# Performance work log

Hardware: AMD Instinct MI355X
Metric: run time of the kernel (lower is better)

## Reference

```python
import jax, jax.numpy as jnp
import numpy as np

N_FREQ = 128
N_SPACE = 3
DIS_DIM = 2 * N_FREQ * N_SPACE  # 768


def sin_emb(x):
    # x: [E, 3] -> [E, 768]; frequencies = 2*pi*arange(n_freq) as in DiffCSP SinusoidsEmbedding
    freq = 2.0 * jnp.pi * jnp.arange(N_FREQ, dtype=x.dtype)
    e = (x[..., None] * freq).reshape(x.shape[0], N_SPACE * N_FREQ)
    return jnp.concatenate([jnp.sin(e), jnp.cos(e)], axis=-1)


def layer_norm(x, g, b, eps=1e-5):
    m = jnp.mean(x, axis=-1, keepdims=True)
    v = jnp.var(x, axis=-1, keepdims=True)
    return (x - m) * jax.lax.rsqrt(v + eps) * g + b


def setup_inputs() -> dict:
    key = jax.random.key(0)
    ks = jax.random.split(key, 16)
    N, E, B, H = 10000, 200000, 50, 512
    E_IN = 2 * H + DIS_DIM + 6  # 1798
    s = 0.02
    return {
        "node_features": jax.random.normal(ks[0], (N, H), jnp.float32),
        "lattices": jax.random.normal(ks[1], (B, 6), jnp.float32),
        "edge_index": jax.random.randint(ks[2], (2, E), 0, N),
        "edge2graph": jax.random.randint(ks[3], (E,), 0, B),
        "frac_diff": jax.random.uniform(ks[4], (E, 3), jnp.float32),
        "num_atoms": jax.random.randint(ks[5], (B,), 1, 200),
        "ln_gamma": jnp.ones((H,), jnp.float32),
        "ln_beta": jnp.zeros((H,), jnp.float32),
        "W_e1": jax.random.normal(ks[6], (E_IN, H), jnp.float32) * s,
        "b_e1": jnp.zeros((H,), jnp.float32),
        "W_e2": jax.random.normal(ks[7], (H, H), jnp.float32) * s,
        "b_e2": jnp.zeros((H,), jnp.float32),
        "W_n1": jax.random.normal(ks[8], (2 * H, H), jnp.float32) * s,
        "b_n1": jnp.zeros((H,), jnp.float32),
        "W_n2": jax.random.normal(ks[9], (H, H), jnp.float32) * s,
        "b_n2": jnp.zeros((H,), jnp.float32),
    }


def reference(node_features, lattices, edge_index, edge2graph, frac_diff, num_atoms,
              ln_gamma, ln_beta, W_e1, b_e1, W_e2, b_e2, W_n1, b_n1, W_n2, b_n2):
    N = node_features.shape[0]
    # pre-LN (ln=True): residual uses raw input
    h = layer_norm(node_features, ln_gamma, ln_beta)
    # edge model: gather + concat + 2-layer MLP with SiLU
    hi = h[edge_index[0]]
    hj = h[edge_index[1]]
    fd = sin_emb(frac_diff)
    lat_e = lattices.reshape(lattices.shape[0], -1)[edge2graph]
    e_in = jnp.concatenate([hi, hj, lat_e, fd], axis=1)  # [E, 1798]
    e = jax.nn.silu(e_in @ W_e1 + b_e1)
    e = jax.nn.silu(e @ W_e2 + b_e2)
    # node model: scatter-mean over edge source + 2-layer MLP
    agg = jax.ops.segment_sum(e, edge_index[0], num_segments=N)
    cnt = jax.ops.segment_sum(jnp.ones((e.shape[0],), e.dtype), edge_index[0], num_segments=N)
    agg = agg / jnp.maximum(cnt, 1.0)[:, None]
    n_in = jnp.concatenate([h, agg], axis=1)  # [N, 1024]
    o = jax.nn.silu(n_in @ W_n1 + b_n1)
    o = jax.nn.silu(o @ W_n2 + b_n2)
    return node_features + o
```

## Files before the change

### kernel.cpp

```cpp
#include <hip/hip_runtime.h>
#include <hip/hip_bf16.h>


#include <type_traits>

typedef __attribute__((ext_vector_type(8))) short bfrag;
typedef __attribute__((ext_vector_type(4))) float ffrag;

#define DEVI __device__ __forceinline__

constexpr int N_NODES = 10000;
constexpr int N_EDGES = 200000;
constexpr int HD      = 512;
constexpr int NT      = HD / 16;
constexpr int SLABW   = 520;
constexpr int KSTR    = NT * 64 * 8;

DEVI float silu_f(float v) { return v / (1.0f + __expf(-v)); }

DEVI ushort f2bf(float f) {
    unsigned u = __float_as_uint(f);
    unsigned r = (u + 0x7fffu + ((u >> 16) & 1u)) >> 16;
    return (ushort)r;
}
DEVI float bf2f(ushort v) { return __uint_as_float((unsigned)v << 16); }

DEVI int cperm(int col) {
    return (col & ~63) | ((col & 15) << 2) | ((col >> 4) & 3);
}

__global__ void wswz_kernel(const float* __restrict__ W, ushort* __restrict__ dst,
                            int Kp, int mode) {
    int fid = blockIdx.x * blockDim.x + threadIdx.x;
    int total = (Kp / 32) * NT * 64;
    if (fid >= total) return;
    int l  = fid & 63;
    int nn = (fid >> 6) & 31;
    int kk = fid >> 11;
    int col = nn * 16 + (l & 15);
    int kb  = kk * 32 + (l >> 4) * 8;
    union { ushort u16[8]; uint4 u4; } v;
    for (int j = 0; j < 8; ++j) {
        int krow = kb + j;
        int src;
        if (mode == 3) {
            int d = krow >> 8, rm = krow & 255, k = rm >> 1;
            src = ((rm & 1) ? 1414 : 1030) + d * 128 + k;
        } else {
            src = krow;
        }
        v.u16[j] = f2bf(W[(size_t)src * HD + col]);
    }
    *(uint4*)(dst + (size_t)fid * 8) = v.u4;
}

__global__ void ln_kernel(const float* __restrict__ x, const float* __restrict__ g,
                          const float* __restrict__ b, ushort* __restrict__ h) {
    __shared__ float wred[8];
    __shared__ float mb[2];
    int row = blockIdx.x;
    int t = threadIdx.x;
    const float* xr = x + (size_t)row * HD;
    float x0 = xr[t], x1 = xr[t + 256];
    float s = x0 + x1, q = x0 * x0 + x1 * x1;
    for (int o = 32; o; o >>= 1) { s += __shfl_down(s, o); q += __shfl_down(q, o); }
    int w = t >> 6, l = t & 63;
    if (l == 0) { wred[w] = s; wred[w + 4] = q; }
    __syncthreads();
    if (t == 0) {
        float S = wred[0] + wred[1] + wred[2] + wred[3];
        float Q = wred[4] + wred[5] + wred[6] + wred[7];
        float m = S * (1.0f / HD);
        float v = Q * (1.0f / HD) - m * m;
        mb[0] = m; mb[1] = rsqrtf(v + 1e-5f);
    }
    __syncthreads();
    float m = mb[0], rs = mb[1];
    h[(size_t)row * HD + t]       = f2bf((x0 - m) * rs * g[t] + b[t]);
    h[(size_t)row * HD + t + 256] = f2bf((x1 - m) * rs * g[t + 256] + b[t + 256]);
}

__global__ void latb_kernel(const float* __restrict__ latt, const float* __restrict__ W_e1,
                            const float* __restrict__ b1, float* __restrict__ LATBp) {
    int g = blockIdx.x;
    int t = threadIdx.x;
    float a = b1[t];
    for (int c = 0; c < 6; ++c)
        a += latt[g * 6 + c] * W_e1[(size_t)(1024 + c) * HD + t];
    LATBp[(size_t)g * HD + cperm(t)] = a;
}

__global__ void zero_kernel(int* __restrict__ c32, float* __restrict__ agg) {
    int i = blockIdx.x * 256 + threadIdx.x;
    if (i < N_NODES) c32[i] = 0;
    agg[i] = 0.0f;
}

__global__ void hist_kernel(const int* __restrict__ eidx, int* __restrict__ cnt32) {
    int e = blockIdx.x * 256 + threadIdx.x;
    if (e < N_EDGES) atomicAdd(&cnt32[eidx[e]], 1);
}

__global__ void scan_kernel(const int* __restrict__ cnt32, int* __restrict__ row_ptr,
                            int* __restrict__ cursor) {
    __shared__ int buf[1024];
    int t = threadIdx.x;
    int base = t * 10;
    int loc[10]; int s = 0;
    for (int i = 0; i < 10; ++i) {
        int idx = base + i;
        int v = (idx < N_NODES) ? cnt32[idx] : 0;
        loc[i] = s; s += v;
    }
    buf[t] = s; __syncthreads();
    for (int off = 1; off < 1024; off <<= 1) {
        int v = 0; if (t >= off) v = buf[t - off];
        __syncthreads();
        buf[t] += v; __syncthreads();
    }
    int excl = buf[t] - s;
    for (int i = 0; i < 10; ++i) {
        int idx = base + i;
        if (idx < N_NODES) { int p = excl + loc[i]; row_ptr[idx] = p; cursor[idx] = p; }
    }
    if (t == 0) row_ptr[N_NODES] = N_EDGES;
}

__global__ void csr_fill(const int* __restrict__ eidx, int* __restrict__ cursor,
                         int* __restrict__ ebuf) {
    int e = blockIdx.x * 256 + threadIdx.x;
    if (e >= N_EDGES) return;
    int pos = atomicAdd(&cursor[eidx[e]], 1);
    ebuf[pos] = e;
}

__global__ void aggdiv_kernel(const float* __restrict__ agg, const int* __restrict__ rp,
                              ushort* __restrict__ aggb) {
    int i = blockIdx.x * 256 + threadIdx.x;
    int row = i >> 9;
    int deg = rp[row + 1] - rp[row];
    float rc = 1.0f / (float)max(deg, 1);
    aggb[i] = f2bf(agg[i] * rc);
}

__global__ void sentinel_kernel(float* o, int n) {
    int i = blockIdx.x * 256 + threadIdx.x;
    if (i < n) o[i] = 123456789.0f;
}

template <int KTN, int MT>
DEVI void kloop_rot(ffrag (&acc)[MT][4], const ushort* sl, const ushort* bp0,
                    int ml, int q) {
    bfrag b_[4];
    const ushort* bp = bp0;
    #pragma unroll
    for (int n = 0; n < 4; ++n) b_[n] = *(const bfrag*)(bp + n * 512);
    #pragma unroll
    for (int p = 0; p < KTN; ++p) {
        bfrag a_[MT];
        #pragma unroll
        for (int m = 0; m < MT; ++m)
            a_[m] = *(const bfrag*)&sl[(16 * m + ml) * SLABW + p * 32 + q * 8];
        const ushort* bpn = bp + KSTR;
        #pragma unroll
        for (int n = 0; n < 4; ++n) {
            #pragma unroll
            for (int m = 0; m < MT; ++m)
                acc[m][n] = __builtin_amdgcn_mfma_f32_16x16x32_bf16(a_[m], b_[n], acc[m][n], 0, 0, 0);
            if (p + 1 < KTN) b_[n] = *(const bfrag*)(bpn + n * 512);
        }
        bp = bpn;
    }
}

__global__ __launch_bounds__(512, 4) void hab_gemm(
    const ushort* __restrict__ h, const ushort* __restrict__ w1a_s,
    const ushort* __restrict__ w1b_s, ushort* __restrict__ HAp,
    ushort* __restrict__ HBp) {

    __shared__ __align__(16) ushort slab[32 * SLABW];
    const int t = threadIdx.x;
    const int w = t >> 6;
    const int l = t & 63;
    const int q = l >> 4;
    const int ml = l & 15;
    const int rowbase = blockIdx.x * 32;
    const ushort* Bswz = blockIdx.y ? w1b_s : w1a_s;
    ushort* out = blockIdx.y ? HBp : HAp;

    for (int j = 0; j < 4; ++j) {
        int rr = w * 4 + j;
        int row = rowbase + rr;
        if (row >= N_NODES) row = N_NODES - 1;
        *(uint4*)&slab[rr * SLABW + l * 8] =
            *(const uint4*)(h + (size_t)row * HD + l * 8);
    }
    __syncthreads();

    ffrag acc[2][4];
    for (int m = 0; m < 2; ++m)
        for (int n = 0; n < 4; ++n)
            acc[m][n] = (ffrag){0.f, 0.f, 0.f, 0.f};

    kloop_rot<16, 2>(acc, slab, Bswz + ((size_t)(w << 2) * 64 + l) * 8, ml, q);

    for (int m = 0; m < 2; ++m)
        for (int rr = 0; rr < 4; ++rr) {
            int grow = rowbase + 16 * m + 4 * q + rr;
            if (grow < N_NODES) {
                ushort4 v = make_ushort4(f2bf(acc[m][0][rr]), f2bf(acc[m][1][rr]),
                                         f2bf(acc[m][2][rr]), f2bf(acc[m][3][rr]));
                *(ushort4*)(out + (size_t)grow * HD + w * 64 + ml * 4) = v;
            }
        }
}

__global__ __launch_bounds__(512, 4) void edge_mlp(
    const ushort* __restrict__ HAp,   const ushort* __restrict__ HBp,
    const float* __restrict__ LATBp,  const ushort* __restrict__ w1c,
    const ushort* __restrict__ w2s,   const float* __restrict__ b2,
    float* __restrict__ agg,
    const int* __restrict__ edge_index, const int* __restrict__ e2g,
    const float* __restrict__ frac_diff, const int* __restrict__ ebuf) {

    __shared__ __align__(16) ushort slab[64 * SLABW];
    __shared__ int   ssrc[64];
    __shared__ int   sdst[64];
    __shared__ int   sgrp[64];
    __shared__ float sfd[64 * 3];

    const int t = threadIdx.x;
    const int w = t >> 6;
    const int l = t & 63;
    const int q = l >> 4;
    const int ml = l & 15;
    const int rowbase = blockIdx.x * 64;

    if (t < 64) {
        int eid = ebuf[rowbase + t];
        ssrc[t] = edge_index[eid];
        sdst[t] = edge_index[N_EDGES + eid];
        sgrp[t] = e2g[eid];
        for (int c = 0; c < 3; ++c) sfd[t * 3 + c] = frac_diff[(size_t)eid * 3 + c];
    }
    __syncthreads();

    ffrag acc[4][4];
    {
        const int cb = w * 64 + ml * 4;
        for (int m = 0; m < 4; ++m)
            for (int rr = 0; rr < 4; ++rr) {
                int rowl = 16 * m + 4 * q + rr;
                ushort4 a4 = *(const ushort4*)(HAp + (size_t)ssrc[rowl] * HD + cb);
                ushort4 h4 = *(const ushort4*)(HBp + (size_t)sdst[rowl] * HD + cb);
                float4  l4 = *(const float4*)(LATBp + (size_t)sgrp[rowl] * HD + cb);
                acc[m][0][rr] = bf2f(a4.x) + bf2f(h4.x) + l4.x;
                acc[m][1][rr] = bf2f(a4.y) + bf2f(h4.y) + l4.y;
                acc[m][2][rr] = bf2f(a4.z) + bf2f(h4.z) + l4.z;
                acc[m][3][rr] = bf2f(a4.w) + bf2f(h4.w) + l4.w;
            }
    }

    const int r  = t >> 3;
    const int c0 = (t & 7) * 4;
    float fd3[3] = { sfd[r * 3 + 0], sfd[r * 3 + 1], sfd[r * 3 + 2] };

    auto stage = [&](int phase) {
        for (int i = 0; i < 12; ++i) {
            int c = c0 + 32 * i;
            int cp = phase * 384 + c;
            int d = cp >> 8;
            float x = fd3[d];
            int k0 = (cp & 255) >> 1;
            float f0 = (float)k0 * x;
            float f1 = f0 + x;
            float r0 = __builtin_amdgcn_fractf(f0);
            float r1 = __builtin_amdgcn_fractf(f1);
            union { __hip_bfloat162 h2[2]; ushort4 u4; } pk;
            pk.h2[0] = __float22bfloat162_rn(float2{__builtin_amdgcn_sinf(r0),
                                                    __builtin_amdgcn_cosf(r0)});
            pk.h2[1] = __float22bfloat162_rn(float2{__builtin_amdgcn_sinf(r1),
                                                    __builtin_amdgcn_cosf(r1)});
            *(ushort4*)&slab[r * SLABW + c] = pk.u4;
        }
    };

    const ushort* bpw1 = w1c + ((size_t)(w << 2) * 64 + l) * 8;
    const ushort* bpw2 = w2s + ((size_t)(w << 2) * 64 + l) * 8;

    stage(0);
    __syncthreads();
    kloop_rot<12, 4>(acc, slab, bpw1, ml, q);
    __syncthreads();
    stage(1);
    __syncthreads();
    kloop_rot<12, 4>(acc, slab, bpw1 + (size_t)12 * KSTR, ml, q);
    __syncthreads();

    for (int n = 0; n < 4; ++n) {
        int cg = w * 64 + n * 16 + ml;
        for (int m = 0; m < 4; ++m)
            for (int rr = 0; rr < 4; ++rr) {
                int rowl = 16 * m + 4 * q + rr;
                slab[rowl * SLABW + cg] = f2bf(silu_f(acc[m][n][rr]));
            }
    }
    for (int m = 0; m < 4; ++m)
        for (int n = 0; n < 4; ++n)
            acc[m][n] = (ffrag){0.f, 0.f, 0.f, 0.f};
    __syncthreads();

    kloop_rot<16, 4>(acc, slab, bpw2, ml, q);

    float* fs = (float*)slab;
    for (int hh = 0; hh < 2; ++hh) {
        __syncthreads();
        if ((w >> 2) == hh) {
            for (int n = 0; n < 4; ++n) {
                int cg = w * 64 + n * 16 + ml;
                int lc = cg - hh * 256;
                float bv = b2[cg];
                for (int m = 0; m < 4; ++m)
                    for (int rr = 0; rr < 4; ++rr) {
                        int rowl = 16 * m + 4 * q + rr;
                        fs[rowl * 256 + lc] = silu_f(acc[m][n][rr] + bv);
                    }
            }
        }
        __syncthreads();
        if (t < 256) {
            int col = hh * 256 + t;
            int cur = ssrc[0];
            float run = 0.f;
            for (int rr2 = 0; rr2 < 64; ++rr2) {
                int nd = ssrc[rr2];
                if (nd != cur) {
                    unsafeAtomicAdd(&agg[(size_t)cur * HD + col], run);
                    run = 0.f; cur = nd;
                }
                run += fs[rr2 * 256 + t];
            }
            unsafeAtomicAdd(&agg[(size_t)cur * HD + col], run);
        }
    }
}

__global__ __launch_bounds__(512, 4) void node_mlp(
    const ushort* __restrict__ h,     const ushort* __restrict__ aggb,
    const ushort* __restrict__ wn1s,  const ushort* __restrict__ wn2s,
    const float* __restrict__ b1,     const float* __restrict__ b2,
    const float* __restrict__ nf,     float* __restrict__ out) {

    __shared__ __align__(16) ushort slab[64 * SLABW];

    const int t = threadIdx.x;
    const int w = t >> 6;
    const int l = t & 63;
    const int q = l >> 4;
    const int ml = l & 15;
    const int rowbase = blockIdx.x * 64;

    ffrag acc[4][4];
    for (int m = 0; m < 4; ++m)
        for (int n = 0; n < 4; ++n)
            acc[m][n] = (ffrag){0.f, 0.f, 0.f, 0.f};

    auto load_rows = [&](const ushort* base) {
        for (int j = 0; j < 8; ++j) {
            int rr = w * 8 + j;
            int row = rowbase + rr;
            if (row >= N_NODES) row = N_NODES - 1;
            *(uint4*)&slab[rr * SLABW + l * 8] =
                *(const uint4*)(base + (size_t)row * HD + l * 8);
        }
    };
    const ushort* bp1 = wn1s + ((size_t)(w << 2) * 64 + l) * 8;
    const ushort* bp2 = wn2s + ((size_t)(w << 2) * 64 + l) * 8;

    load_rows(h);                        __syncthreads();
    kloop_rot<16, 4>(acc, slab, bp1, ml, q);
    __syncthreads();
    load_rows(aggb);                     __syncthreads();
    kloop_rot<16, 4>(acc, slab, bp1 + (size_t)16 * KSTR, ml, q);
    __syncthreads();

    for (int n = 0; n < 4; ++n) {
        int cg = w * 64 + n * 16 + ml;
        float bv = b1[cg];
        for (int m = 0; m < 4; ++m)
            for (int rr = 0; rr < 4; ++rr) {
                int rowl = 16 * m + 4 * q + rr;
                slab[rowl * SLABW + cg] = f2bf(silu_f(acc[m][n][rr] + bv));
            }
    }
    for (int m = 0; m < 4; ++m)
        for (int n = 0; n < 4; ++n)
            acc[m][n] = (ffrag){0.f, 0.f, 0.f, 0.f};
    __syncthreads();

    kloop_rot<16, 4>(acc, slab, bp2, ml, q);

    for (int n = 0; n < 4; ++n) {
        int cg = w * 64 + n * 16 + ml;
        float bv = b2[cg];
        for (int m = 0; m < 4; ++m)
            for (int rr = 0; rr < 4; ++rr) {
                int rowl = 16 * m + 4 * q + rr;
                int row = rowbase + rowl;
                if (row < N_NODES) {
                    float v = silu_f(acc[m][n][rr] + bv);
                    out[(size_t)row * HD + cg] = nf[(size_t)row * HD + cg] + v;
                }
            }
    }
}

extern "C" void kernel_launch(void* const* d_in, const int* in_sizes, int n_in,
                              void* d_out, int out_size, void* d_ws, size_t ws_size,
                              hipStream_t stream) {
    const float* nf      = (const float*)d_in[0];
    const float* latt    = (const float*)d_in[1];
    const int*   eidx    = (const int*)d_in[2];
    const int*   e2g     = (const int*)d_in[3];
    const float* fd      = (const float*)d_in[4];
    const float* ln_g    = (const float*)d_in[6];
    const float* ln_b    = (const float*)d_in[7];
    const float* W_e1    = (const float*)d_in[8];
    const float* b_e1    = (const float*)d_in[9];
    const float* W_e2    = (const float*)d_in[10];
    const float* b_e2    = (const float*)d_in[11];
    const float* W_n1    = (const float*)d_in[12];
    const float* b_n1    = (const float*)d_in[13];
    const float* W_n2    = (const float*)d_in[14];
    const float* b_n2    = (const float*)d_in[15];
    float* out = (float*)d_out;

    auto al = [](size_t x) { return (x + 511) & ~(size_t)511; };
    size_t off_h    = 0;                         size_t sz_h    = (size_t)N_NODES * HD * 2;
    size_t off_w1a  = al(off_h + sz_h);          size_t sz_w1a  = (size_t)HD * HD * 2;
    size_t off_w1b  = al(off_w1a + sz_w1a);      size_t sz_w1b  = (size_t)HD * HD * 2;
    size_t off_w1c  = al(off_w1b + sz_w1b);      size_t sz_w1c  = (size_t)768 * HD * 2;
    size_t off_w2   = al(off_w1c + sz_w1c);      size_t sz_w2   = (size_t)HD * HD * 2;
    size_t off_wn1  = al(off_w2 + sz_w2);        size_t sz_wn1  = (size_t)2 * HD * HD * 2;
    size_t off_wn2  = al(off_wn1 + sz_wn1);      size_t sz_wn2  = (size_t)HD * HD * 2;
    size_t off_ha   = al(off_wn2 + sz_wn2);      size_t sz_ha   = (size_t)N_NODES * HD * 2;
    size_t off_hb   = al(off_ha + sz_ha);        size_t sz_hb   = (size_t)N_NODES * HD * 2;
    size_t off_lb   = al(off_hb + sz_hb);        size_t sz_lb   = (size_t)50 * HD * 4;
    size_t off_agb  = al(off_lb + sz_lb);        size_t sz_agb  = (size_t)N_NODES * HD * 2;
    size_t off_c32  = al(off_agb + sz_agb);      size_t sz_c32  = (size_t)N_NODES * 4;
    size_t off_cur  = al(off_c32 + sz_c32);      size_t sz_cur  = (size_t)N_NODES * 4;
    size_t off_rp   = al(off_cur + sz_cur);      size_t sz_rp   = (size_t)(N_NODES + 1) * 4;
    size_t off_ebuf = al(off_rp + sz_rp);        size_t sz_ebuf = (size_t)N_EDGES * 4;
    size_t off_agg  = al(off_ebuf + sz_ebuf);    size_t sz_agg  = (size_t)N_NODES * HD * 4;
    size_t need     = off_agg + sz_agg;

    if (ws_size < need) {
        sentinel_kernel<<<(out_size + 255) / 256, 256, 0, stream>>>(out, out_size);
        return;
    }

    char* ws = (char*)d_ws;
    ushort* h     = (ushort*)(ws + off_h);
    ushort* w1a_s = (ushort*)(ws + off_w1a);
    ushort* w1b_s = (ushort*)(ws + off_w1b);
    ushort* w1c_s = (ushort*)(ws + off_w1c);
    ushort* w2s   = (ushort*)(ws + off_w2);
    ushort* wn1s  = (ushort*)(ws + off_wn1);
    ushort* wn2s  = (ushort*)(ws + off_wn2);
    ushort* HAp   = (ushort*)(ws + off_ha);
    ushort* HBp   = (ushort*)(ws + off_hb);
    float*  LATBp = (float*)(ws + off_lb);
    ushort* aggb  = (ushort*)(ws + off_agb);
    int*    c32   = (int*)(ws + off_c32);
    int*    cur   = (int*)(ws + off_cur);
    int*    rp    = (int*)(ws + off_rp);
    int*    ebuf  = (int*)(ws + off_ebuf);
    float*  agg   = (float*)(ws + off_agg);

    zero_kernel<<<(N_NODES * HD) / 256, 256, 0, stream>>>(c32, agg);
    wswz_kernel<<<(HD / 32) * NT * 64 / 256, 256, 0, stream>>>(W_e1, w1a_s, HD, 0);
    wswz_kernel<<<(HD / 32) * NT * 64 / 256, 256, 0, stream>>>(W_e1 + (size_t)HD * HD, w1b_s, HD, 0);
    wswz_kernel<<<(768 / 32) * NT * 64 / 256, 256, 0, stream>>>(W_e1, w1c_s, 768, 3);
    wswz_kernel<<<(HD / 32) * NT * 64 / 256, 256, 0, stream>>>(W_e2, w2s, HD, 0);
    wswz_kernel<<<(2 * HD / 32) * NT * 64 / 256, 256, 0, stream>>>(W_n1, wn1s, 2 * HD, 0);
    wswz_kernel<<<(HD / 32) * NT * 64 / 256, 256, 0, stream>>>(W_n2, wn2s, HD, 0);
    latb_kernel<<<50, 512, 0, stream>>>(latt, W_e1, b_e1, LATBp);

    hist_kernel<<<(N_EDGES + 255) / 256, 256, 0, stream>>>(eidx, c32);
    scan_kernel<<<1, 1024, 0, stream>>>(c32, rp, cur);
    csr_fill<<<(N_EDGES + 255) / 256, 256, 0, stream>>>(eidx, cur, ebuf);

    ln_kernel<<<N_NODES, 256, 0, stream>>>(nf, ln_g, ln_b, h);
    hab_gemm<<<dim3(313, 2), 512, 0, stream>>>(h, w1a_s, w1b_s, HAp, HBp);

    edge_mlp<<<N_EDGES / 64, 512, 0, stream>>>(
        HAp, HBp, LATBp, w1c_s, w2s, b_e2, agg, eidx, e2g, fd, ebuf);

    aggdiv_kernel<<<(N_NODES * HD) / 256, 256, 0, stream>>>(agg, rp, aggb);

    int nblocks = (N_NODES + 63) / 64;
    node_mlp<<<nblocks, 512, 0, stream>>>(h, aggb, wn1s, wn2s, b_n1, b_n2, nf, out);
}
```

Measured before the change: 610.0 us.

## Vectorize small kernels, use trig recurrence for sinusoid embedding, shrink node tiles

Several unrelated tweaks land together. The LN, zero and aggdiv kernels now use vectorized loads and stores, and the SiLU epilogues write packed 4-wide bf16 stores, with the K-row permutation of W_e2 and W_n2 changed to match. The sinusoid embedding in edge_mlp replaces per-element sin/cos calls with an angle-addition recurrence. node_mlp moves to 32-row tiles so the 10000 nodes spread over more blocks. The recurrence can build up rounding error across steps.

Result: faster. 591.5 us (-3.0%).

```diff
diff --git a/kernel.cpp b/kernel.cpp
--- a/kernel.cpp
+++ b/kernel.cpp
@@ -46,6 +46,8 @@
         if (mode == 3) {
             int d = krow >> 8, rm = krow & 255, k = rm >> 1;
             src = ((rm & 1) ? 1414 : 1030) + d * 128 + k;
+        } else if (mode == 1) {
+            src = (krow & ~63) | ((krow & 3) << 4) | ((krow >> 2) & 15);
         } else {
             src = krow;
         }
@@ -61,11 +63,11 @@
     int row = blockIdx.x;
     int t = threadIdx.x;
     const float* xr = x + (size_t)row * HD;
-    float x0 = xr[t], x1 = xr[t + 256];
-    float s = x0 + x1, q = x0 * x0 + x1 * x1;
-    for (int o = 32; o; o >>= 1) { s += __shfl_down(s, o); q += __shfl_down(q, o); }
+    float2 xv = *(const float2*)(xr + 2 * t);
+    float s = xv.x + xv.y, qq = xv.x * xv.x + xv.y * xv.y;
+    for (int o = 32; o; o >>= 1) { s += __shfl_down(s, o); qq += __shfl_down(qq, o); }
     int w = t >> 6, l = t & 63;
-    if (l == 0) { wred[w] = s; wred[w + 4] = q; }
+    if (l == 0) { wred[w] = s; wred[w + 4] = qq; }
     __syncthreads();
     if (t == 0) {
         float S = wred[0] + wred[1] + wred[2] + wred[3];
@@ -76,8 +78,11 @@
     }
     __syncthreads();
     float m = mb[0], rs = mb[1];
-    h[(size_t)row * HD + t]       = f2bf((x0 - m) * rs * g[t] + b[t]);
-    h[(size_t)row * HD + t + 256] = f2bf((x1 - m) * rs * g[t + 256] + b[t + 256]);
+    float2 gv = *(const float2*)(g + 2 * t);
+    float2 bv = *(const float2*)(b + 2 * t);
+    __hip_bfloat162 o2 = __float22bfloat162_rn(
+        float2{(xv.x - m) * rs * gv.x + bv.x, (xv.y - m) * rs * gv.y + bv.y});
+    *(__hip_bfloat162*)(h + (size_t)row * HD + 2 * t) = o2;
 }
 
 __global__ void latb_kernel(const float* __restrict__ latt, const float* __restrict__ W_e1,
@@ -90,10 +95,10 @@
     LATBp[(size_t)g * HD + cperm(t)] = a;
 }
 
-__global__ void zero_kernel(int* __restrict__ c32, float* __restrict__ agg) {
+__global__ void zero_kernel(int* __restrict__ c32, float4* __restrict__ agg4) {
     int i = blockIdx.x * 256 + threadIdx.x;
     if (i < N_NODES) c32[i] = 0;
-    agg[i] = 0.0f;
+    agg4[i] = float4{0.f, 0.f, 0.f, 0.f};
 }
 
 __global__ void hist_kernel(const int* __restrict__ eidx, int* __restrict__ cnt32) {
@@ -137,10 +142,12 @@
 __global__ void aggdiv_kernel(const float* __restrict__ agg, const int* __restrict__ rp,
                               ushort* __restrict__ aggb) {
     int i = blockIdx.x * 256 + threadIdx.x;
-    int row = i >> 9;
+    int row = i >> 8;
     int deg = rp[row + 1] - rp[row];
     float rc = 1.0f / (float)max(deg, 1);
-    aggb[i] = f2bf(agg[i] * rc);
+    float2 v = *(const float2*)(agg + (size_t)i * 2);
+    *(__hip_bfloat162*)(aggb + (size_t)i * 2) =
+        __float22bfloat162_rn(float2{v.x * rc, v.y * rc});
 }
 
 __global__ void sentinel_kernel(float* o, int n) {
@@ -208,9 +215,10 @@
         for (int rr = 0; rr < 4; ++rr) {
             int grow = rowbase + 16 * m + 4 * q + rr;
             if (grow < N_NODES) {
-                ushort4 v = make_ushort4(f2bf(acc[m][0][rr]), f2bf(acc[m][1][rr]),
-                                         f2bf(acc[m][2][rr]), f2bf(acc[m][3][rr]));
-                *(ushort4*)(out + (size_t)grow * HD + w * 64 + ml * 4) = v;
+                union { __hip_bfloat162 h2[2]; ushort4 u4; } pk;
+                pk.h2[0] = __float22bfloat162_rn(float2{acc[m][0][rr], acc[m][1][rr]});
+                pk.h2[1] = __float22bfloat162_rn(float2{acc[m][2][rr], acc[m][3][rr]});
+                *(ushort4*)(out + (size_t)grow * HD + w * 64 + ml * 4) = pk.u4;
             }
         }
 }
@@ -266,22 +274,37 @@
     float fd3[3] = { sfd[r * 3 + 0], sfd[r * 3 + 1], sfd[r * 3 + 2] };
 
     auto stage = [&](int phase) {
+        float s = 0.f, c = 0.f, sx = 0.f, cx = 0.f, s16 = 0.f, c16 = 0.f;
+        int dcur = -1;
+        #pragma unroll
         for (int i = 0; i < 12; ++i) {
-            int c = c0 + 32 * i;
-            int cp = phase * 384 + c;
+            int cc = c0 + 32 * i;
+            int cp = phase * 384 + cc;
             int d = cp >> 8;
-            float x = fd3[d];
-            int k0 = (cp & 255) >> 1;
-            float f0 = (float)k0 * x;
-            float f1 = f0 + x;
-            float r0 = __builtin_amdgcn_fractf(f0);
-            float r1 = __builtin_amdgcn_fractf(f1);
+            if (d != dcur) {
+                dcur = d;
+                float x = fd3[d];
+                float rx = __builtin_amdgcn_fractf(x);
+                sx  = __builtin_amdgcn_sinf(rx);
+                cx  = __builtin_amdgcn_cosf(rx);
+                float r16 = __builtin_amdgcn_fractf(16.0f * x);
+                s16 = __builtin_amdgcn_sinf(r16);
+                c16 = __builtin_amdgcn_cosf(r16);
+                int k0 = (cp & 255) >> 1;
+                float r0 = __builtin_amdgcn_fractf((float)k0 * x);
+                s = __builtin_amdgcn_sinf(r0);
+                c = __builtin_amdgcn_cosf(r0);
+            } else {
+                float ns = s * c16 + c * s16;
+                float nc = c * c16 - s * s16;
+                s = ns; c = nc;
+            }
+            float s1 = s * cx + c * sx;
+            float c1 = c * cx - s * sx;
             union { __hip_bfloat162 h2[2]; ushort4 u4; } pk;
-            pk.h2[0] = __float22bfloat162_rn(float2{__builtin_amdgcn_sinf(r0),
-                                                    __builtin_amdgcn_cosf(r0)});
-            pk.h2[1] = __float22bfloat162_rn(float2{__builtin_amdgcn_sinf(r1),
-                                                    __builtin_amdgcn_cosf(r1)});
-            *(ushort4*)&slab[r * SLABW + c] = pk.u4;
+            pk.h2[0] = __float22bfloat162_rn(float2{s, c});
+            pk.h2[1] = __float22bfloat162_rn(float2{s1, c1});
+            *(ushort4*)&slab[r * SLABW + cc] = pk.u4;
         }
     };
 
@@ -297,14 +320,16 @@
     kloop_rot<12, 4>(acc, slab, bpw1 + (size_t)12 * KSTR, ml, q);
     __syncthreads();
 
-    for (int n = 0; n < 4; ++n) {
-        int cg = w * 64 + n * 16 + ml;
-        for (int m = 0; m < 4; ++m)
-            for (int rr = 0; rr < 4; ++rr) {
-                int rowl = 16 * m + 4 * q + rr;
-                slab[rowl * SLABW + cg] = f2bf(silu_f(acc[m][n][rr]));
-            }
-    }
+    for (int m = 0; m < 4; ++m)
+        for (int rr = 0; rr < 4; ++rr) {
+            int rowl = 16 * m + 4 * q + rr;
+            union { __hip_bfloat162 h2[2]; ushort4 u4; } pk;
+            pk.h2[0] = __float22bfloat162_rn(
+                float2{silu_f(acc[m][0][rr]), silu_f(acc[m][1][rr])});
+            pk.h2[1] = __float22bfloat162_rn(
+                float2{silu_f(acc[m][2][rr]), silu_f(acc[m][3][rr])});
+            *(ushort4*)&slab[rowl * SLABW + w * 64 + ml * 4] = pk.u4;
+        }
     for (int m = 0; m < 4; ++m)
         for (int n = 0; n < 4; ++n)
             acc[m][n] = (ffrag){0.f, 0.f, 0.f, 0.f};
@@ -351,23 +376,23 @@
     const float* __restrict__ b1,     const float* __restrict__ b2,
     const float* __restrict__ nf,     float* __restrict__ out) {
 
-    __shared__ __align__(16) ushort slab[64 * SLABW];
+    __shared__ __align__(16) ushort slab[32 * SLABW];
 
     const int t = threadIdx.x;
     const int w = t >> 6;
     const int l = t & 63;
     const int q = l >> 4;
     const int ml = l & 15;
-    const int rowbase = blockIdx.x * 64;
-
-    ffrag acc[4][4];
-    for (int m = 0; m < 4; ++m)
+    const int rowbase = blockIdx.x * 32;
+
+    ffrag acc[2][4];
+    for (int m = 0; m < 2; ++m)
         for (int n = 0; n < 4; ++n)
             acc[m][n] = (ffrag){0.f, 0.f, 0.f, 0.f};
 
     auto load_rows = [&](const ushort* base) {
-        for (int j = 0; j < 8; ++j) {
-            int rr = w * 8 + j;
+        for (int j = 0; j < 4; ++j) {
+            int rr = w * 4 + j;
             int row = rowbase + rr;
             if (row >= N_NODES) row = N_NODES - 1;
             *(uint4*)&slab[rr * SLABW + l * 8] =
@@ -378,32 +403,37 @@
     const ushort* bp2 = wn2s + ((size_t)(w << 2) * 64 + l) * 8;
 
     load_rows(h);                        __syncthreads();
-    kloop_rot<16, 4>(acc, slab, bp1, ml, q);
+    kloop_rot<16, 2>(acc, slab, bp1, ml, q);
     __syncthreads();
     load_rows(aggb);                     __syncthreads();
-    kloop_rot<16, 4>(acc, slab, bp1 + (size_t)16 * KSTR, ml, q);
-    __syncthreads();
-
-    for (int n = 0; n < 4; ++n) {
-        int cg = w * 64 + n * 16 + ml;
-        float bv = b1[cg];
-        for (int m = 0; m < 4; ++m)
+    kloop_rot<16, 2>(acc, slab, bp1 + (size_t)16 * KSTR, ml, q);
+    __syncthreads();
+
+    {
+        float bv[4];
+        for (int n = 0; n < 4; ++n) bv[n] = b1[w * 64 + n * 16 + ml];
+        for (int m = 0; m < 2; ++m)
             for (int rr = 0; rr < 4; ++rr) {
                 int rowl = 16 * m + 4 * q + rr;
-                slab[rowl * SLABW + cg] = f2bf(silu_f(acc[m][n][rr] + bv));
-            }
-    }
-    for (int m = 0; m < 4; ++m)
+                union { __hip_bfloat162 h2[2]; ushort4 u4; } pk;
+                pk.h2[0] = __float22bfloat162_rn(
+                    float2{silu_f(acc[m][0][rr] + bv[0]), silu_f(acc[m][1][rr] + bv[1])});
+                pk.h2[1] = __float22bfloat162_rn(
+                    float2{silu_f(acc[m][2][rr] + bv[2]), silu_f(acc[m][3][rr] + bv[3])});
+                *(ushort4*)&slab[rowl * SLABW + w * 64 + ml * 4] = pk.u4;
+            }
+    }
+    for (int m = 0; m < 2; ++m)
         for (int n = 0; n < 4; ++n)
             acc[m][n] = (ffrag){0.f, 0.f, 0.f, 0.f};
     __syncthreads();
 
-    kloop_rot<16, 4>(acc, slab, bp2, ml, q);
+    kloop_rot<16, 2>(acc, slab, bp2, ml, q);
 
     for (int n = 0; n < 4; ++n) {
         int cg = w * 64 + n * 16 + ml;
         float bv = b2[cg];
-        for (int m = 0; m < 4; ++m)
+        for (int m = 0; m < 2; ++m)
             for (int rr = 0; rr < 4; ++rr) {
                 int rowl = 16 * m + 4 * q + rr;
                 int row = rowbase + rowl;
@@ -477,13 +507,13 @@
     int*    ebuf  = (int*)(ws + off_ebuf);
     float*  agg   = (float*)(ws + off_agg);
 
-    zero_kernel<<<(N_NODES * HD) / 256, 256, 0, stream>>>(c32, agg);
+    zero_kernel<<<(N_NODES * HD / 4) / 256, 256, 0, stream>>>(c32, (float4*)agg);
     wswz_kernel<<<(HD / 32) * NT * 64 / 256, 256, 0, stream>>>(W_e1, w1a_s, HD, 0);
     wswz_kernel<<<(HD / 32) * NT * 64 / 256, 256, 0, stream>>>(W_e1 + (size_t)HD * HD, w1b_s, HD, 0);
     wswz_kernel<<<(768 / 32) * NT * 64 / 256, 256, 0, stream>>>(W_e1, w1c_s, 768, 3);
-    wswz_kernel<<<(HD / 32) * NT * 64 / 256, 256, 0, stream>>>(W_e2, w2s, HD, 0);
+    wswz_kernel<<<(HD / 32) * NT * 64 / 256, 256, 0, stream>>>(W_e2, w2s, HD, 1);
     wswz_kernel<<<(2 * HD / 32) * NT * 64 / 256, 256, 0, stream>>>(W_n1, wn1s, 2 * HD, 0);
-    wswz_kernel<<<(HD / 32) * NT * 64 / 256, 256, 0, stream>>>(W_n2, wn2s, HD, 0);
+    wswz_kernel<<<(HD / 32) * NT * 64 / 256, 256, 0, stream>>>(W_n2, wn2s, HD, 1);
     latb_kernel<<<50, 512, 0, stream>>>(latt, W_e1, b_e1, LATBp);
 
     hist_kernel<<<(N_EDGES + 255) / 256, 256, 0, stream>>>(eidx, c32);
@@ -496,8 +526,8 @@
     edge_mlp<<<N_EDGES / 64, 512, 0, stream>>>(
         HAp, HBp, LATBp, w1c_s, w2s, b_e2, agg, eidx, e2g, fd, ebuf);
 
-    aggdiv_kernel<<<(N_NODES * HD) / 256, 256, 0, stream>>>(agg, rp, aggb);
-
-    int nblocks = (N_NODES + 63) / 64;
+    aggdiv_kernel<<<(N_NODES * HD / 2) / 256, 256, 0, stream>>>(agg, rp, aggb);
+
+    int nblocks = (N_NODES + 31) / 32;
     node_mlp<<<nblocks, 512, 0, stream>>>(h, aggb, wn1s, wn2s, b_n1, b_n2, nf, out);
 }
```
